# Kernel tuning notes

Measured on AMD Instinct MI355X. Metric: run time of the kernel, lower is better.

## Reference

```python
import jax, jax.numpy as jnp
import numpy as np

N = 12  # mmse_block_size
REAL_SIZE = N * (N + 1) // 2  # 78: diag + strict lower
IMAG_SIZE = N * (N - 1) // 2  # 66: strict lower only
ROWS, COLS = jnp.tril_indices(N)        # row-major (i, j<=i) matches torch loop order
ROWS_S, COLS_S = jnp.tril_indices(N, -1)  # strict lower, row-major, matches imag loop
DIAG_MASK = jnp.eye(N, dtype=bool)


def _mlp(x, W1, b1, W2, b2, W3, b3):
    h = jax.nn.relu(x @ W1 + b1)
    h = jax.nn.relu(h @ W2 + b2)
    return h @ W3 + b3


def _cholesky_outer(flat):
    # flat: [B, REAL_SIZE + IMAG_SIZE] -> [B, N, N] complex, L @ L^H
    B = flat.shape[0]
    L_real = jnp.zeros((B, N, N), flat.dtype).at[:, ROWS, COLS].set(flat[:, :REAL_SIZE])
    L_real = jnp.where(DIAG_MASK, jax.nn.softplus(L_real), L_real)
    L_imag = jnp.zeros((B, N, N), flat.dtype).at[:, ROWS_S, COLS_S].set(
        flat[:, REAL_SIZE:REAL_SIZE + IMAG_SIZE])
    L = L_real + 1j * L_imag
    return jnp.einsum('bij,bkj->bik', L, jnp.conj(L))


def setup_inputs() -> dict:
    key = jax.random.key(0)
    ks = jax.random.split(key, 13)
    L, H, OUT = 4096, 64, REAL_SIZE + IMAG_SIZE
    sc = lambda k, shp, fan: (jax.random.normal(k, shp, jnp.float32) / np.sqrt(fan))
    return {
        'channel_stats': jax.random.normal(ks[0], (8192, L), jnp.float32),
        'WC1': sc(ks[1], (L, H), L), 'bC1': jnp.zeros((H,), jnp.float32),
        'WC2': sc(ks[2], (H, H), H), 'bC2': jnp.zeros((H,), jnp.float32),
        'WC3': sc(ks[3], (H, OUT), H), 'bC3': jnp.zeros((OUT,), jnp.float32),
        'WR1': sc(ks[4], (L, H), L), 'bR1': jnp.zeros((H,), jnp.float32),
        'WR2': sc(ks[5], (H, H), H), 'bR2': jnp.zeros((H,), jnp.float32),
        'WR3': sc(ks[6], (H, OUT), H), 'bR3': jnp.zeros((OUT,), jnp.float32),
    }


def reference(channel_stats, WC1, bC1, WC2, bC2, WC3, bC3,
              WR1, bR1, WR2, bR2, WR3, bR3):
    C_flat = _mlp(channel_stats, WC1, bC1, WC2, bC2, WC3, bC3)
    R_flat = _mlp(channel_stats, WR1, bR1, WR2, bR2, WR3, bR3)
    C = _cholesky_outer(C_flat)
    R = _cholesky_outer(R_flat)
    return C, R
```

## Files before the change

### kernel.cpp

```cpp
#include <hip/hip_runtime.h>
#include <stdint.h>

#define M_ROWS 8192
#define K_DIM  4096
#define OUTD   144
#define PLANE  1179648
#define NT     32

typedef __attribute__((ext_vector_type(4))) float  float4v;
typedef __attribute__((ext_vector_type(8))) short  short8v;
typedef __attribute__((ext_vector_type(4))) short  short4v;

#define AS1 __attribute__((address_space(1)))
#define AS3 __attribute__((address_space(3)))

static __device__ __forceinline__ unsigned short f2bf(float f) {
    unsigned int u = __builtin_bit_cast(unsigned int, f);
    u += 0x7FFFu + ((u >> 16) & 1u);
    return (unsigned short)(u >> 16);
}

__global__ __launch_bounds__(256) void wt_kernel(
    const float* __restrict__ WC1, const float* __restrict__ WR1,
    unsigned short* __restrict__ Wt) {
    __shared__ float tile[64][65];
    const float* src = (blockIdx.y == 0) ? WC1 : WR1;
    const int k0 = blockIdx.x * 64;
    const int t = threadIdx.x;
    const int j = t & 63, q = t >> 6;
#pragma unroll
    for (int p = 0; p < 16; ++p) {
        int i = p * 4 + q;
        tile[i][j] = src[(size_t)(k0 + i) * 64 + j];
    }
    __syncthreads();
#pragma unroll
    for (int p = 0; p < 16; ++p) {
        int n = p * 4 + q;
        Wt[(size_t)(blockIdx.y * 64 + n) * K_DIM + k0 + j] = f2bf(tile[j][n]);
    }
}


#define GLOADB(CUR_, KK_)                                                     \
    do {                                                                      \
        unsigned short* d0_ = Bsm_ + (CUR_) * 16384 + w * 512;                \
        _Pragma("unroll")                                                     \
        for (int p_ = 0; p_ < 4; ++p_) {                                      \
            __builtin_amdgcn_global_load_lds(                                 \
                (const AS1 void*)(const void*)(bsrc0 + (size_t)p_ * 32 * K_DIM + (KK_)), \
                (AS3 void*)(void*)(d0_ + p_ * 4096), 16, 0, 0);               \
        }                                                                     \
    } while (0)

#define MF(CUR_)                                                              \
    do {                                                                      \
        _Pragma("unroll")                                                     \
        for (int ks = 0; ks < 4; ++ks) {                                      \
            short8v a_ = *(const short8v*)&Asm_[(CUR_) * 2176 + m * 136 + ks * 32 + q * 8]; \
            int sb_ = (ks * 4 + q) ^ (m & 7);                                 \
            short8v b_ = *(const short8v*)&Bsm_[(CUR_) * 16384 + (w * 16 + m) * 128 + sb_ * 8]; \
            acc = __builtin_amdgcn_mfma_f32_16x16x32_bf16(a_, b_, acc, 0, 0, 0); \
        }                                                                     \
    } while (0)

__global__ __launch_bounds__(512, 4) void fused_kernel(
    const float* __restrict__ X, const unsigned short* __restrict__ Wt,
    const float* __restrict__ bC1, const float* __restrict__ bR1,
    const float* __restrict__ WC2, const float* __restrict__ bC2,
    const float* __restrict__ WR2, const float* __restrict__ bR2,
    const float* __restrict__ WC3, const float* __restrict__ bC3,
    const float* __restrict__ WR3, const float* __restrict__ bR3,
    unsigned short* __restrict__ OUT) {
    __shared__ __align__(16) char smem[74240];
    unsigned short* Asm_ = (unsigned short*)smem;
    unsigned short* Bsm_ = Asm_ + 2 * 16 * 136;
    float* hs  = (float*)smem;
    float* W2s = hs + 16 * 132;
    float* fl  = W2s;

    const int tid  = threadIdx.x;
    const int lane = tid & 63;
    const int w    = tid >> 6;
    const int r0   = blockIdx.x * 16;
    const int m    = lane & 15, q = lane >> 4;
    const int ar   = tid >> 5, akc = tid & 31;

    float4v acc = {0.f, 0.f, 0.f, 0.f};

    const int sub  = lane >> 4;
    const int gseg = (lane & 15) ^ (((w & 1) * 4 + sub) & 7);
    const unsigned short* bsrc0 =
        Wt + (size_t)(w * 4 + sub) * K_DIM + gseg * 8;
    const float* xp = X + (size_t)(r0 + ar) * K_DIM + akc * 4;
    unsigned short* awp = Asm_ + ar * 136 + akc * 4;

    GLOADB(0, 0);
    float4 xa = *(const float4*)(xp + 0);

#pragma unroll 2
    for (int t = 0; t < NT; ++t) {
        const int cur = t & 1;
        asm volatile("s_waitcnt vmcnt(0)" ::: "memory");
        short4v s_;
        s_.x = (short)f2bf(xa.x); s_.y = (short)f2bf(xa.y);
        s_.z = (short)f2bf(xa.z); s_.w = (short)f2bf(xa.w);
        *(short4v*)(awp + cur * 2176) = s_;
        asm volatile("s_waitcnt lgkmcnt(0)" ::: "memory");
        __builtin_amdgcn_s_barrier();
        __builtin_amdgcn_sched_barrier(0);
        if (t + 1 < NT) {
            GLOADB(cur ^ 1, (t + 1) * 128);
            xa = *(const float4*)(xp + (t + 1) * 128);
        }
        MF(cur);
    }
    __syncthreads();

    {
        const int c = w * 16 + m;
        const float bv = (c < 64) ? bC1[c] : bR1[c - 64];
#pragma unroll
        for (int i = 0; i < 4; ++i) {
            int r = q * 4 + i;
            float v = acc[i] + bv; v = v > 0.f ? v : 0.f;
            hs[r * 132 + c] = v;
        }
    }
#pragma unroll
    for (int p = 0; p < 4; ++p) {
        int fi = p * 512 + tid;
        int k = fi >> 5, c4 = fi & 31;
        int c = c4 * 4;
        const float* wsrc = (c < 64) ? (WC2 + (size_t)k * 64 + c)
                                     : (WR2 + (size_t)k * 64 + (c - 64));
        *(float4*)&W2s[k * 128 + c] = *(const float4*)wsrc;
    }
    __syncthreads();

    const int rg = tid >> 5;
    const int cg = tid & 31;
    const int koff2 = (cg < 16) ? 0 : 64;
    float acc2[4];
    {
        int c = cg * 4;
        const float* bsrc = (c < 64) ? (bC2 + c) : (bR2 + (c - 64));
#pragma unroll
        for (int j = 0; j < 4; ++j) acc2[j] = bsrc[j];
    }
    for (int k = 0; k < 64; ++k) {
        float4 wv = *(const float4*)&W2s[k * 128 + cg * 4];
        float a = hs[rg * 132 + koff2 + k];
        acc2[0] += a * wv.x; acc2[1] += a * wv.y;
        acc2[2] += a * wv.z; acc2[3] += a * wv.w;
    }
    float4 h2v;
    h2v.x = acc2[0] > 0.f ? acc2[0] : 0.f;
    h2v.y = acc2[1] > 0.f ? acc2[1] : 0.f;
    h2v.z = acc2[2] > 0.f ? acc2[2] : 0.f;
    h2v.w = acc2[3] > 0.f ? acc2[3] : 0.f;
    __syncthreads();
    *(float4*)&hs[rg * 132 + cg * 4] = h2v;
    __syncthreads();

#pragma unroll 1
    for (int pass = 0; pass < 3; ++pass) {
        int c = pass * 128 + cg * 4;
        if (c < 288) {
            const int brn = (c >= 144);
            const int cl = c - (brn ? 144 : 0);
            const float* W3 = brn ? WR3 : WC3;
            const float* b3 = brn ? bR3 : bC3;
            const int ko = brn ? 64 : 0;
            float a3[4];
#pragma unroll
            for (int j = 0; j < 4; ++j) a3[j] = b3[cl + j];
            for (int k = 0; k < 64; ++k) {
                float4 wv = *(const float4*)(W3 + (size_t)k * OUTD + cl);
                float a = hs[rg * 132 + ko + k];
                a3[0] += a * wv.x; a3[1] += a * wv.y;
                a3[2] += a * wv.z; a3[3] += a * wv.w;
            }
            float4 v; v.x = a3[0]; v.y = a3[1]; v.z = a3[2]; v.w = a3[3];
            *(float4*)&fl[rg * 288 + c] = v;
        }
    }
    __syncthreads();

    if (tid < 384) {
        int r = tid / 24, rem = tid % 24;
        int brn = rem / 12, ii = rem % 12;
        float* f = &fl[r * 288 + brn * 144];
        int d = ii * (ii + 1) / 2 + ii;
        float xv = f[d];
        f[d] = (xv > 20.f) ? xv : log1pf(expf(xv));
    }
    __syncthreads();

    unsigned int* O32 = (unsigned int*)OUT;
    for (int task = tid; task < 16 * 2 * 78; task += 512) {
        int r = task / 156, rem = task % 156;
        int brn = rem / 78, p = rem % 78;
        int i = 0;
        while (p >= (i + 1) * (i + 2) / 2) ++i;
        int j = p - i * (i + 1) / 2;
        const float* f = &fl[r * 288 + brn * 144];
        const float* g = f + 78;
        const int ti = i * (i + 1) / 2, tj = j * (j + 1) / 2;
        const int si = i * (i - 1) / 2, sj = j * (j - 1) / 2;
        float re = 0.f, im = 0.f;
        for (int k = 0; k <= j; ++k) {
            float ar_ = f[ti + k];
            float ai  = (k == i) ? 0.f : g[si + k];
            float br_ = f[tj + k];
            float bi  = (k == j) ? 0.f : g[sj + k];
            re += ar_ * br_ + ai * bi;
            im += ai * br_ - ar_ * bi;
        }
        unsigned int reb = (unsigned int)f2bf(re);
        unsigned int imb = (unsigned int)f2bf(im);
        unsigned int imn = (unsigned int)f2bf(-im);
        size_t base = brn ? (size_t)PLANE : 0;
        size_t q1 = (size_t)(r0 + r) * 144 + (size_t)(i * 12 + j);
        O32[base + q1] = imb | (reb << 16);
        if (i != j) {
            size_t q2 = (size_t)(r0 + r) * 144 + (size_t)(j * 12 + i);
            O32[base + q2] = imn | (reb << 16);
        }
    }
}

extern "C" void kernel_launch(void* const* d_in, const int* in_sizes, int n_in,
                              void* d_out, int out_size, void* d_ws, size_t ws_size,
                              hipStream_t stream) {
    const float* X   = (const float*)d_in[0];
    const float* WC1 = (const float*)d_in[1];
    const float* bC1 = (const float*)d_in[2];
    const float* WC2 = (const float*)d_in[3];
    const float* bC2 = (const float*)d_in[4];
    const float* WC3 = (const float*)d_in[5];
    const float* bC3 = (const float*)d_in[6];
    const float* WR1 = (const float*)d_in[7];
    const float* bR1 = (const float*)d_in[8];
    const float* WR2 = (const float*)d_in[9];
    const float* bR2 = (const float*)d_in[10];
    const float* WR3 = (const float*)d_in[11];
    const float* bR3 = (const float*)d_in[12];

    unsigned short* Wt = (unsigned short*)d_ws;
    unsigned short* OUT = (unsigned short*)d_out;

    wt_kernel<<<dim3(64, 2), 256, 0, stream>>>(WC1, WR1, Wt);
    fused_kernel<<<M_ROWS / 16, 512, 0, stream>>>(
        X, Wt, bC1, bR1, WC2, bC2, WR2, bR2, WC3, bC3, WR3, bR3, OUT);
}
```

Before: 260.8 us.

## Prepack W1 into MFMA fragment layout and load B directly into registers

```diff
diff --git a/kernel.cpp b/kernel.cpp
--- a/kernel.cpp
+++ b/kernel.cpp
@@ -9,10 +9,6 @@
 
 typedef __attribute__((ext_vector_type(4))) float  float4v;
 typedef __attribute__((ext_vector_type(8))) short  short8v;
-typedef __attribute__((ext_vector_type(4))) short  short4v;
-
-#define AS1 __attribute__((address_space(1)))
-#define AS3 __attribute__((address_space(3)))
 
 static __device__ __forceinline__ unsigned short f2bf(float f) {
     unsigned int u = __builtin_bit_cast(unsigned int, f);
@@ -27,41 +23,60 @@
     const float* src = (blockIdx.y == 0) ? WC1 : WR1;
     const int k0 = blockIdx.x * 64;
     const int t = threadIdx.x;
-    const int j = t & 63, q = t >> 6;
+    const int j = t & 63, qq = t >> 6;
 #pragma unroll
     for (int p = 0; p < 16; ++p) {
-        int i = p * 4 + q;
+        int i = p * 4 + qq;
         tile[i][j] = src[(size_t)(k0 + i) * 64 + j];
     }
     __syncthreads();
+    const int tt  = blockIdx.x >> 1;
+    const int ksb = (blockIdx.x & 1) * 2;
 #pragma unroll
     for (int p = 0; p < 16; ++p) {
-        int n = p * 4 + q;
-        Wt[(size_t)(blockIdx.y * 64 + n) * K_DIM + k0 + j] = f2bf(tile[j][n]);
-    }
-}
-
-
-#define GLOADB(CUR_, KK_)                                                     \
-    do {                                                                      \
-        unsigned short* d0_ = Bsm_ + (CUR_) * 16384 + w * 512;                \
-        _Pragma("unroll")                                                     \
-        for (int p_ = 0; p_ < 4; ++p_) {                                      \
-            __builtin_amdgcn_global_load_lds(                                 \
-                (const AS1 void*)(const void*)(bsrc0 + (size_t)p_ * 32 * K_DIM + (KK_)), \
-                (AS3 void*)(void*)(d0_ + p_ * 4096), 16, 0, 0);               \
-        }                                                                     \
-    } while (0)
-
-#define MF(CUR_)                                                              \
-    do {                                                                      \
-        _Pragma("unroll")                                                     \
-        for (int ks = 0; ks < 4; ++ks) {                                      \
-            short8v a_ = *(const short8v*)&Asm_[(CUR_) * 2176 + m * 136 + ks * 32 + q * 8]; \
-            int sb_ = (ks * 4 + q) ^ (m & 7);                                 \
-            short8v b_ = *(const short8v*)&Bsm_[(CUR_) * 16384 + (w * 16 + m) * 128 + sb_ * 8]; \
-            acc = __builtin_amdgcn_mfma_f32_16x16x32_bf16(a_, b_, acc, 0, 0, 0); \
-        }                                                                     \
+        int c = p * 256 + t;
+        int e = c & 7, m = (c >> 3) & 15, q = (c >> 7) & 3;
+        int ks_l = (c >> 9) & 1, w_l = (c >> 10) & 3;
+        int kp = ks_l * 32 + q * 8 + e;
+        int np = w_l * 16 + m;
+        int wg = blockIdx.y * 4 + w_l;
+        size_t dst = ((size_t)(wg * 32 + tt) * 4 + (ksb + ks_l)) * 512
+                   + q * 128 + m * 8 + e;
+        Wt[dst] = f2bf(tile[kp][np]);
+    }
+}
+
+
+#define ISSUE_B(T_, B0_, B1_, B2_, B3_)                          \
+    do { const unsigned short* bp_ = bpw + (size_t)(T_) * 2048;  \
+         B0_ = *(const short8v*)(bp_ + 0 * 512);                 \
+         B1_ = *(const short8v*)(bp_ + 1 * 512);                 \
+         B2_ = *(const short8v*)(bp_ + 2 * 512);                 \
+         B3_ = *(const short8v*)(bp_ + 3 * 512); } while (0)
+
+#define ISSUE_A(T_, XL_, XH_)                                    \
+    do { const float* ap_ = xpw + (size_t)(T_) * 128;            \
+         XL_ = *(const float4*)(ap_);                            \
+         XH_ = *(const float4*)(ap_ + 4); } while (0)
+
+#define STORE_A(XL_, XH_, BUF_)                                        \
+    do { short8v s_;                                                   \
+         s_[0] = (short)f2bf((XL_).x); s_[1] = (short)f2bf((XL_).y);   \
+         s_[2] = (short)f2bf((XL_).z); s_[3] = (short)f2bf((XL_).w);   \
+         s_[4] = (short)f2bf((XH_).x); s_[5] = (short)f2bf((XH_).y);   \
+         s_[6] = (short)f2bf((XH_).z); s_[7] = (short)f2bf((XH_).w);   \
+         *(short8v*)(Asm_ + (BUF_) * 2048 + (w * 64 + lane) * 8) = s_; } while (0)
+
+#define MFR(BUF_, B0_, B1_, B2_, B3_)                                          \
+    do { const unsigned short* ab_ = Asm_ + (BUF_) * 2048 + lane * 8;          \
+         short8v a0_ = *(const short8v*)(ab_ + 0 * 512);                       \
+         short8v a1_ = *(const short8v*)(ab_ + 1 * 512);                       \
+         short8v a2_ = *(const short8v*)(ab_ + 2 * 512);                       \
+         short8v a3_ = *(const short8v*)(ab_ + 3 * 512);                       \
+         acc = __builtin_amdgcn_mfma_f32_16x16x32_bf16(a0_, B0_, acc, 0, 0, 0);\
+         acc = __builtin_amdgcn_mfma_f32_16x16x32_bf16(a1_, B1_, acc, 0, 0, 0);\
+         acc = __builtin_amdgcn_mfma_f32_16x16x32_bf16(a2_, B2_, acc, 0, 0, 0);\
+         acc = __builtin_amdgcn_mfma_f32_16x16x32_bf16(a3_, B3_, acc, 0, 0, 0);\
     } while (0)
 
 __global__ __launch_bounds__(512, 4) void fused_kernel(
@@ -72,9 +87,8 @@
     const float* __restrict__ WC3, const float* __restrict__ bC3,
     const float* __restrict__ WR3, const float* __restrict__ bR3,
     unsigned short* __restrict__ OUT) {
-    __shared__ __align__(16) char smem[74240];
+    __shared__ __align__(16) char smem[41216];
     unsigned short* Asm_ = (unsigned short*)smem;
-    unsigned short* Bsm_ = Asm_ + 2 * 16 * 136;
     float* hs  = (float*)smem;
     float* W2s = hs + 16 * 132;
     float* fl  = W2s;
@@ -84,36 +98,36 @@
     const int w    = tid >> 6;
     const int r0   = blockIdx.x * 16;
     const int m    = lane & 15, q = lane >> 4;
-    const int ar   = tid >> 5, akc = tid & 31;
 
     float4v acc = {0.f, 0.f, 0.f, 0.f};
 
-    const int sub  = lane >> 4;
-    const int gseg = (lane & 15) ^ (((w & 1) * 4 + sub) & 7);
-    const unsigned short* bsrc0 =
-        Wt + (size_t)(w * 4 + sub) * K_DIM + gseg * 8;
-    const float* xp = X + (size_t)(r0 + ar) * K_DIM + akc * 4;
-    unsigned short* awp = Asm_ + ar * 136 + akc * 4;
-
-    GLOADB(0, 0);
-    float4 xa = *(const float4*)(xp + 0);
-
-#pragma unroll 2
-    for (int t = 0; t < NT; ++t) {
-        const int cur = t & 1;
-        asm volatile("s_waitcnt vmcnt(0)" ::: "memory");
-        short4v s_;
-        s_.x = (short)f2bf(xa.x); s_.y = (short)f2bf(xa.y);
-        s_.z = (short)f2bf(xa.z); s_.w = (short)f2bf(xa.w);
-        *(short4v*)(awp + cur * 2176) = s_;
+    const unsigned short* bpw = Wt + (size_t)w * 32 * 2048 + lane * 8;
+    const float* xpw = X + (size_t)(r0 + m) * K_DIM + w * 32 + q * 8;
+    const bool stager = (w < 4);
+
+    short8v b00, b01, b02, b03, b10, b11, b12, b13;
+    float4 xl0, xh0, xl1, xh1;
+
+    ISSUE_B(0, b00, b01, b02, b03);
+    if (stager) ISSUE_A(0, xl0, xh0);
+
+#pragma unroll 1
+    for (int t = 0; t < NT; t += 2) {
+        if (stager) { STORE_A(xl0, xh0, 0); ISSUE_A(t + 1, xl1, xh1); }
         asm volatile("s_waitcnt lgkmcnt(0)" ::: "memory");
         __builtin_amdgcn_s_barrier();
         __builtin_amdgcn_sched_barrier(0);
-        if (t + 1 < NT) {
-            GLOADB(cur ^ 1, (t + 1) * 128);
-            xa = *(const float4*)(xp + (t + 1) * 128);
-        }
-        MF(cur);
+        ISSUE_B(t + 1, b10, b11, b12, b13);
+        MFR(0, b00, b01, b02, b03);
+        if (stager) {
+            STORE_A(xl1, xh1, 1);
+            if (t + 2 < NT) ISSUE_A(t + 2, xl0, xh0);
+        }
+        asm volatile("s_waitcnt lgkmcnt(0)" ::: "memory");
+        __builtin_amdgcn_s_barrier();
+        __builtin_amdgcn_sched_barrier(0);
+        if (t + 2 < NT) ISSUE_B(t + 2, b00, b01, b02, b03);
+        MFR(1, b10, b11, b12, b13);
     }
     __syncthreads();
 
```

New measurement: 261.3 us. No clear change (+0.2%).
